# Kernel optimization log

Hardware: AMD Instinct MI355X
Metric: run time of the kernel (lower is better)

Reference implementation:

```python
import jax, jax.numpy as jnp
import numpy as np

D_Z, D_X, K, T = 128, 64, 16, 2048
JITTER = 1e-4
# Tsit5 Butcher tableau. diffrax.diffeqsolve with the default ConstantStepSize
# controller and dt0 = t_curr - t_prev takes exactly ONE Tsit5 step per interval,
# so a single explicit Tsit5 step reproduces the original math.
A21 = 0.161
A31, A32 = -0.008480655492356989, 0.335480655492357
A41, A42, A43 = 2.8971530571054935, -6.359448489975075, 4.3622954328695815
A51, A52, A53, A54 = 5.325864828439257, -11.748883564062828, 7.4955393428898365, -0.09249506636175525
A61, A62, A63, A64, A65 = 5.86145544294642, -12.92096931784711, 8.159367898576159, -0.071584973281401, -0.028269050394068383
B1, B2, B3, B4, B5, B6 = 0.09646076681806523, 0.01, 0.4798896504144996, 1.379008574103742, -3.290069515436081, 2.324710524099774


def setup_inputs() -> dict:
    key = jax.random.key(0)
    ks = jax.random.split(key, 8)
    xs = jax.random.normal(ks[0], (T, D_X), jnp.float32)
    ts = jnp.arange(T, dtype=jnp.float32) * 0.01  # strictly increasing observation times
    expected_s = jax.nn.softmax(jax.random.normal(ks[1], (T, K), jnp.float32), axis=-1)
    mu_0 = jax.random.normal(ks[2], (D_Z,), jnp.float32)
    P_0 = jnp.eye(D_Z, dtype=jnp.float32)
    # stable continuous dynamics: small random part, negative diagonal shift
    A_s = 0.02 * jax.random.normal(ks[3], (K, D_Z, D_Z), jnp.float32) - 0.5 * jnp.eye(D_Z, dtype=jnp.float32)
    b_s = 0.1 * jax.random.normal(ks[4], (K, D_Z), jnp.float32)
    Q_s_chol = 0.1 + 0.1 * jax.random.uniform(ks[5], (K, D_Z), dtype=jnp.float32)
    C = jax.random.normal(ks[6], (D_X, D_Z), jnp.float32) / jnp.sqrt(jnp.float32(D_Z))
    R = 0.1 * jnp.eye(D_X, dtype=jnp.float32)
    return dict(xs=xs, ts=ts, expected_s=expected_s, mu_0=mu_0, P_0=P_0,
                A_s=A_s, b_s=b_s, Q_s_chol=Q_s_chol, C=C, R=R)


def _ode_func(state, s_prob, A_s, b_s, Q_s_chol):
    # state packs [mu (D_Z), P.flatten() (D_Z*D_Z)]
    mu, P = state[:D_Z], state[D_Z:].reshape(D_Z, D_Z)
    w = s_prob / jnp.sum(s_prob)  # jnp.average(..., weights=s_prob) semantics
    drift = jnp.einsum('k,kij,j->i', w, A_s, mu) + w @ b_s
    eA = jnp.einsum('k,kij->ij', w, A_s)
    eQ = jnp.diag(w @ (Q_s_chol ** 2))  # weighted avg of diag(Q_chol)^2
    dP = eA @ P + P @ eA.T + eQ
    return jnp.concatenate([drift, dP.reshape(-1)])


def _kf_update(mu, P, x, C, R):
    y = x - C @ mu
    S = C @ P @ C.T + R + JITTER * jnp.eye(R.shape[0], dtype=P.dtype)
    cho = jax.scipy.linalg.cho_factor(S)
    Kg = jax.scipy.linalg.cho_solve(cho, C @ P).T
    mu_u = mu + Kg @ y
    P_u = P - Kg @ C @ P
    return mu_u, 0.5 * (P_u + P_u.T)


def reference(xs, ts, expected_s, mu_0, P_0, A_s, b_s, Q_s_chol, C, R):
    mu0u, P0u = _kf_update(mu_0, P_0, xs[0], C, R)

    def step(carry, inp):
        mu_prev, P_prev, t_prev = carry
        x, t, s = inp
        y0 = jnp.concatenate([mu_prev, P_prev.reshape(-1)])
        f = lambda st: _ode_func(st, s, A_s, b_s, Q_s_chol)

        def integrate(_):
            h = t - t_prev
            k1 = f(y0)
            k2 = f(y0 + h * (A21 * k1))
            k3 = f(y0 + h * (A31 * k1 + A32 * k2))
            k4 = f(y0 + h * (A41 * k1 + A42 * k2 + A43 * k3))
            k5 = f(y0 + h * (A51 * k1 + A52 * k2 + A53 * k3 + A54 * k4))
            k6 = f(y0 + h * (A61 * k1 + A62 * k2 + A63 * k3 + A64 * k4 + A65 * k5))
            return y0 + h * (B1 * k1 + B2 * k2 + B3 * k3 + B4 * k4 + B5 * k5 + B6 * k6)

        state_pred = jax.lax.cond(t > t_prev, integrate, lambda _: y0, None)
        mu_pr, P_pr = state_pred[:D_Z], state_pred[D_Z:].reshape(D_Z, D_Z)
        mu_u, P_u = _kf_update(mu_pr, P_pr, x, C, R)
        return (mu_u, P_u, t), (mu_u, P_u)

    _, (mu_f, P_f) = jax.lax.scan(step, (mu0u, P0u, ts[0]), (xs[1:], ts[1:], expected_s[1:]))
    mu_filt = jnp.concatenate([mu0u[None], mu_f], axis=0)  # (T, D_Z)
    P_filt = jnp.concatenate([P0u[None], P_f], axis=0)  # (T, D_Z, D_Z)
    return mu_filt, P_filt
```

## Files before the change

### kernel.cpp

```cpp
#include <hip/hip_runtime.h>
#include <math.h>

#define DZ 128
#define DX 64
#define KMIX 16
#define JITTER_C 1e-4f
#define MS (DZ*DZ)
#define ESZ (4*MS + 2*DZ)
#define NCH 256
#define NT 1024
#define SCN (5*MS + 256)

#define SP   0
#define SX   (1*MS)
#define SX2  (2*MS)
#define SX2T (3*MS)
#define SQ   (4*MS)

template<int M, int N, int K, int MODE, bool DUAL>
__device__ void mm_(const float* __restrict__ At, const float* __restrict__ B,
                    float* __restrict__ out, const float* __restrict__ aux,
                    float* __restrict__ outT, float e1 = 0.f)
{
    __syncthreads();
    const int tid = threadIdx.x;
    constexpr int TM = M/32, TN = N/32;
    const int tx = tid & 31, ty = tid >> 5;
    const int i0 = ty*TM, j0 = tx*TN;
    float acc[TM*TN];
#pragma unroll
    for (int e = 0; e < TM*TN; ++e) acc[e] = 0.f;
    auto body = [&](int k) {
        const float* ar = At + k*M + i0;
        const float* br = B + k*N + j0;
        float av[TM], bv[TN];
        if constexpr (TM == 2) {
            float2 t = *reinterpret_cast<const float2*>(ar);
            av[0]=t.x; av[1]=t.y;
        } else {
#pragma unroll
            for (int a = 0; a < TM; a += 4) {
                float4 t = *reinterpret_cast<const float4*>(ar + a);
                av[a]=t.x; av[a+1]=t.y; av[a+2]=t.z; av[a+3]=t.w;
            }
        }
        if constexpr (TN == 2) {
            float2 t = *reinterpret_cast<const float2*>(br);
            bv[0]=t.x; bv[1]=t.y;
        } else {
#pragma unroll
            for (int b = 0; b < TN; b += 4) {
                float4 t = *reinterpret_cast<const float4*>(br + b);
                bv[b]=t.x; bv[b+1]=t.y; bv[b+2]=t.z; bv[b+3]=t.w;
            }
        }
#pragma unroll
        for (int a = 0; a < TM; ++a)
#pragma unroll
            for (int b = 0; b < TN; ++b)
                acc[a*TN+b] = fmaf(av[a], bv[b], acc[a*TN+b]);
    };
    const int off = (tid >> 6) * (K >> 4);
#pragma unroll 8
    for (int k = off; k < K; ++k) body(k);
#pragma unroll 8
    for (int k = 0; k < off; ++k) body(k);
#pragma unroll
    for (int a = 0; a < TM; ++a) {
#pragma unroll
        for (int b = 0; b < TN; ++b) {
            const int row = i0+a, col = j0+b;
            const int idx = row*N + col;
            float v = acc[a*TN+b];
            if constexpr (MODE == 1) v += out[idx];
            else if constexpr (MODE == 2) v = aux[idx] - v;
            else if constexpr (MODE == 3) v += aux[idx];
            else if constexpr (MODE == 4) { v += e1*aux[idx]; if (row==col) v += 1.f; }
            out[idx] = v;
            acc[a*TN+b] = v;
        }
    }
    if constexpr (DUAL) {
#pragma unroll
        for (int b = 0; b < TN; ++b) {
#pragma unroll
            for (int a = 0; a < TM; a += 4) {
                float4 v = make_float4(acc[(a)*TN+b], acc[(a+1)*TN+b], acc[(a+2)*TN+b], acc[(a+3)*TN+b]);
                *reinterpret_cast<float4*>(outT + (j0+b)*M + i0 + a) = v;
            }
        }
    }
    __syncthreads();
}

template<int M, int K, int MODE>
__device__ void mv_(const float* __restrict__ At, const float* __restrict__ v,
                    float* __restrict__ out, const float* __restrict__ aux)
{
    __syncthreads();
    const int tid = threadIdx.x;
    constexpr int TPR = NT / M;
    constexpr int CH  = K / TPR;
    const int r  = tid / TPR;
    const int sg = tid % TPR;
    const int k0 = sg * CH;
    float s = 0.f;
#pragma unroll
    for (int k = 0; k < CH; ++k)
        s = fmaf(At[(k0 + k)*M + r], v[k0 + k], s);
#pragma unroll
    for (int o = 1; o < TPR; o <<= 1) s += __shfl_xor(s, o);
    if (sg == 0) {
        float rr;
        if constexpr (MODE == 0) rr = s;
        else if constexpr (MODE == 1) rr = aux[r] + s;
        else rr = aux[r] - s;
        out[r] = rr;
    }
    __syncthreads();
}

__device__ void trans_g(const float* __restrict__ src, float* __restrict__ dst,
                        float* __restrict__ Lb)
{
    __syncthreads();
    for (int e = threadIdx.x; e < MS; e += NT) {
        int i = e >> 7, j = e & 127;
        Lb[(i << 7) + (j ^ (i & 31))] = src[e];
    }
    __syncthreads();
    for (int e = threadIdx.x; e < MS; e += NT) {
        int a = e >> 7, b = e & 127;
        dst[e] = Lb[(b << 7) + (a ^ (b & 31))];
    }
    __syncthreads();
}

__device__ void gj64_spd(float* __restrict__ A, float* __restrict__ st)
{
    const int tid = threadIdx.x;
    for (int p = 0; p < DX; p += 4) {
        __syncthreads();
        if (tid < 64) {
#pragma unroll
            for (int b = 0; b < 4; ++b) st[tid*4+b] = A[tid*DX + p + b];
        } else if (tid < 128) {
            int j = tid - 64;
#pragma unroll
            for (int b = 0; b < 4; ++b) st[256 + b*64 + j] = A[(p+b)*DX + j];
        }
        __syncthreads();
        float Dm[16], Di[16];
#pragma unroll
        for (int a = 0; a < 4; ++a)
#pragma unroll
            for (int b = 0; b < 4; ++b) {
                Dm[a*4+b] = st[(p+a)*4 + b];
                Di[a*4+b] = (a==b) ? 1.f : 0.f;
            }
#pragma unroll
        for (int q = 0; q < 4; ++q) {
            float rp = 1.f / Dm[q*4+q];
#pragma unroll
            for (int j = 0; j < 4; ++j) { Dm[q*4+j] *= rp; Di[q*4+j] *= rp; }
#pragma unroll
            for (int i = 0; i < 4; ++i) {
                if (i == q) continue;
                float f = Dm[i*4+q];
#pragma unroll
                for (int j = 0; j < 4; ++j) { Dm[i*4+j] = fmaf(-f, Dm[q*4+j], Dm[i*4+j]); Di[i*4+j] = fmaf(-f, Di[q*4+j], Di[i*4+j]); }
            }
        }
        for (int e = tid; e < DX*DX; e += NT) {
            const int i = e >> 6, j = e & 63;
            const bool iP = (i >= p) && (i < p+4);
            const bool jP = (j >= p) && (j < p+4);
            float o;
            if (iP && jP) {
                o = Di[(i-p)*4 + (j-p)];
            } else if (iP) {
                const int a = i - p;
                o = Di[a*4+0]*st[256+0*64+j] + Di[a*4+1]*st[256+1*64+j]
                  + Di[a*4+2]*st[256+2*64+j] + Di[a*4+3]*st[256+3*64+j];
            } else {
                float Ei[4];
#pragma unroll
                for (int b = 0; b < 4; ++b)
                    Ei[b] = st[i*4+0]*Di[0*4+b] + st[i*4+1]*Di[1*4+b]
                          + st[i*4+2]*Di[2*4+b] + st[i*4+3]*Di[3*4+b];
                if (jP) o = -Ei[j-p];
                else    o = A[e] - (Ei[0]*st[256+0*64+j] + Ei[1]*st[256+1*64+j]
                                  + Ei[2]*st[256+2*64+j] + Ei[3]*st[256+3*64+j]);
            }
            A[e] = o;
        }
    }
    __syncthreads();
}

__device__ void gj128_piv(float* __restrict__ A, float* __restrict__ pc, float* __restrict__ pr,
                          int* __restrict__ rec, int* __restrict__ ipv1)
{
    __syncthreads();
    const int tid = threadIdx.x;
    for (int p = 0; p < DZ; ++p) {
        if (tid < 64) {
            float best = -1.f; int bi = p;
            for (int i = tid; i < DZ; i += 64) {
                float v = (i >= p) ? fabsf(A[i*DZ + p]) : -2.f;
                if (v > best) { best = v; bi = i; }
            }
            for (int off = 32; off > 0; off >>= 1) {
                float ob = __shfl_xor(best, off);
                int obi = __shfl_xor(bi, off);
                if (ob > best) { best = ob; bi = obi; }
            }
            if (tid == 0) { rec[p] = bi; ipv1[0] = bi; }
        }
        __syncthreads();
        const int r = ipv1[0];
        if (r != p) {
            for (int j = tid; j < DZ; j += NT) { float t = A[p*DZ+j]; A[p*DZ+j] = A[r*DZ+j]; A[r*DZ+j] = t; }
            __syncthreads();
        }
        if (tid < DZ) { pc[tid] = A[tid*DZ + p]; pr[tid] = A[p*DZ + tid]; }
        __syncthreads();
        const float rp = 1.f / pr[p];
        for (int e = tid; e < MS; e += NT) {
            const int i = e >> 7, j = e & 127;
            const float pv = pr[j] * rp;
            float o;
            if (i == p) o = (j == p) ? rp : pv;
            else { const float fc = pc[i]; o = (j == p) ? (-fc*rp) : (A[e] - fc*pv); }
            A[e] = o;
        }
        __syncthreads();
    }
    for (int p = DZ - 1; p >= 0; --p) {
        const int r = rec[p];
        if (r != p) {
            for (int i = tid; i < DZ; i += NT) { float t = A[i*DZ+p]; A[i*DZ+p] = A[i*DZ+r]; A[i*DZ+r] = t; }
            __syncthreads();
        }
    }
    __syncthreads();
}

__device__ void phase1_dev(int k,
    const float* __restrict__ A_s, const float* __restrict__ b_s,
    const float* __restrict__ Qch, const float* __restrict__ es, const float* __restrict__ ts,
    float* sx, float* sx2, float* sx2t, float* sq,
    float* L0, float* L1,
    float* W16, float* ebv, float* eqv, float* vvv, float* cvec,
    float g1, float g2, float g3, float g4)
{
    const int tid = threadIdx.x;
    const float h = ts[k] - ts[k-1];
    if (h <= 0.f) {
        __syncthreads();
        for (int e = tid; e < MS; e += NT) {
            int i = e >> 7, j = e & 127;
            L0[e] = (i==j) ? 1.f : 0.f;
            sq[e] = 0.f;
        }
        if (tid < DZ) cvec[tid] = 0.f;
        __syncthreads();
        return;
    }
    __syncthreads();
    if (tid < KMIX) W16[tid] = es[(size_t)k*KMIX + tid];
    __syncthreads();
    if (tid == 0) {
        float s = 0.f;
        for (int m = 0; m < KMIX; ++m) s += W16[m];
        float inv = 1.f/s;
        for (int m = 0; m < KMIX; ++m) W16[m] *= inv;
    }
    __syncthreads();
    if (tid < DZ) {
        float eb = 0.f, eq = 0.f;
        for (int m = 0; m < KMIX; ++m) {
            float wm = W16[m];
            eb = fmaf(wm, b_s[m*DZ+tid], eb);
            float qc = Qch[m*DZ+tid];
            eq = fmaf(wm, qc*qc, eq);
        }
        ebv[tid] = eb; eqv[tid] = eq;
    }
    const int tx = tid & 31, ty = tid >> 5;
    const int i0 = ty*4, j0 = tx*4;
    float t16[16];
#pragma unroll
    for (int e = 0; e < 16; ++e) t16[e] = 0.f;
    {
        const int mq = (tid >> 6) & (KMIX - 1);
        for (int mi = 0; mi < KMIX; ++mi) {
            int m = mi + mq; if (m >= KMIX) m -= KMIX;
            float wm = W16[m];
            const float* Am = A_s + (size_t)m * MS;
#pragma unroll
            for (int a = 0; a < 4; ++a) {
                float4 p0 = *reinterpret_cast<const float4*>(&Am[(i0+a)*DZ + j0]);
                t16[a*4+0]=fmaf(wm,p0.x,t16[a*4+0]); t16[a*4+1]=fmaf(wm,p0.y,t16[a*4+1]);
                t16[a*4+2]=fmaf(wm,p0.z,t16[a*4+2]); t16[a*4+3]=fmaf(wm,p0.w,t16[a*4+3]);
            }
        }
    }
#pragma unroll
    for (int a = 0; a < 4; ++a)
#pragma unroll
        for (int b = 0; b < 4; ++b) {
            float v = h * t16[a*4+b];
            L1[(i0+a)*DZ + (j0+b)] = v;
            sx[(i0+a)*DZ + (j0+b)] = v;
            L0[(j0+b)*DZ + (i0+a)] = v;
        }
    __syncthreads();
    {
        float gg[5]; gg[1]=g1; gg[2]=g2; gg[3]=g3; gg[4]=g4;
        if (tid < DZ) vvv[tid] = ebv[tid];
        float creg = (tid < DZ) ? g1 * ebv[tid] : 0.f;
        __syncthreads();
        for (int m = 1; m <= 3; ++m) {
            float vn = 0.f;
            if (tid < DZ)
                for (int kk = 0; kk < DZ; ++kk)
                    vn = fmaf(L0[kk*DZ + tid], vvv[kk], vn);
            __syncthreads();
            if (tid < DZ) vvv[tid] = vn;
            creg = fmaf(gg[m+1], vn, creg);
            __syncthreads();
        }
        if (tid < DZ) cvec[tid] = h * creg;
    }
    mm_<128,128,128,0,true>(L0, L1, sx2, nullptr, sx2t);
    for (int e = tid; e < MS; e += NT) {
        int j = e >> 7, i = e & 127;
        float xt = L0[e];
        float w1  = g2*sx[e] + g3*sx2[e];
        float w1t = g2*xt    + g3*sx2t[e];
        float vq = w1*eqv[i] + eqv[j]*w1t;
        if (i == j) vq += g1*eqv[j];
        sq[e] = h * vq;
        L1[e] = g3*xt + ((i==j) ? g2 : 0.f);
    }
    __syncthreads();
    mm_<128,128,128,4,false>(sx2, L1, L0, L0, nullptr, g1);
}

#define SHARED_DECLS \
    __shared__ __align__(16) float L0[MS]; \
    __shared__ __align__(16) float L1[MS]; \
    __shared__ __align__(16) float SL[DX*DX]; \
    __shared__ __align__(16) float GJB[520]; \
    __shared__ float V0[DZ],V1[DZ],V2[DZ],V3[DZ],V4[DZ],V5[DZ]; \
    __shared__ float r64s[DX], u64s[DX]; \
    __shared__ float W16[KMIX], ebv[DZ], eqv[DZ], vvv[DZ], cvec[DZ]; \
    __shared__ float GJc[DZ], GJr[DZ]; \
    __shared__ int REC[DZ]; __shared__ int IPV1[1];

__global__ __launch_bounds__(NT) void kf_prep(
    const float* __restrict__ Cm, const float* __restrict__ Rm,
    const float* __restrict__ mu0, const float* __restrict__ P0,
    const float* __restrict__ xs,
    float* Ct, float* Rj, float* Rji, float* mu0u, float* p0u, float* scr)
{
    SHARED_DECLS
    const int tid = threadIdx.x;
    for (int i = tid; i < DZ*DX; i += NT) { int z = i>>6, m = i&63; Ct[i] = Cm[m*DZ + z]; }
    for (int i = tid; i < DX*DX; i += NT) {
        int a = i>>6, b = i&63;
        float v = Rm[i] + ((a==b) ? JITTER_C : 0.f);
        Rj[i] = v; SL[i] = v;
    }
    gj64_spd(SL, GJB);
    for (int i = tid; i < DX*DX; i += NT) Rji[i] = SL[i];
    float* z  = scr + SX;
    float* cp = scr + SX + DZ*DX;
    float* kt = scr + SX2;
    mm_<128,64,128,0,true>(P0, Ct, z, nullptr, cp);
    mm_<64,64,128,3,false>(Ct, z, SL, Rj, nullptr);
    gj64_spd(SL, GJB);
    mm_<64,128,64,0,false>(SL, cp, kt, nullptr, nullptr);
    mv_<64,128,2>(Ct, mu0, r64s, xs);
    mv_<128,64,1>(kt, r64s, mu0u, mu0);
    mm_<128,128,64,2,false>(kt, cp, p0u, P0, nullptr);
    __syncthreads();
    for (int e = tid; e < MS; e += NT) L0[e] = p0u[e];
    __syncthreads();
    for (int e = tid; e < MS; e += NT) {
        int i = e>>7, j = e&127;
        p0u[e] = 0.5f * (L0[e] + L0[j*DZ + i]);
    }
}

__global__ __launch_bounds__(NT) void kf_passA(
    const float* __restrict__ A_s, const float* __restrict__ b_s,
    const float* __restrict__ Qch, const float* __restrict__ es,
    const float* __restrict__ ts, const float* __restrict__ xs,
    const float* __restrict__ Ct, const float* __restrict__ Rj,
    const float* __restrict__ Rji,
    const float* __restrict__ mu0u, const float* __restrict__ p0u,
    float* elems, float* scr, int T, int LCH,
    float g1, float g2, float g3, float g4)
{
    SHARED_DECLS
    const int c = blockIdx.x, tid = threadIdx.x;
    float* sc = scr + (size_t)c * SCN;
    float* R = elems + (size_t)c * ESZ;
    float* RAs = R; float* RAts = R+MS; float* RCs = R+2*MS; float* RJs = R+3*MS;
    float* Rbs = R+4*MS; float* Rhs = R+4*MS+DZ;
    int eBeg = c*LCH, eEnd = (c*LCH + LCH < T) ? (c*LCH + LCH) : T;
    if (eBeg >= eEnd && c != 0) {
        for (int e = tid; e < MS; e += NT) {
            int i = e>>7, j = e&127; float id = (i==j)?1.f:0.f;
            RAs[e]=id; RAts[e]=id; RCs[e]=0.f; RJs[e]=0.f;
        }
        if (tid < DZ) { Rbs[tid]=0.f; Rhs[tid]=0.f; }
        return;
    }
    if (c == 0) {
        for (int e = tid; e < MS; e += NT) { RAs[e]=0.f; RCs[e]=p0u[e]; RJs[e]=0.f; }
        if (tid < DZ) { V0[tid]=mu0u[tid]; V5[tid]=0.f; }
        eBeg = 1;
    } else {
        for (int e = tid; e < MS; e += NT) {
            int i = e>>7, j = e&127;
            RAs[e] = (i==j)?1.f:0.f; RCs[e]=0.f; RJs[e]=0.f;
        }
        if (tid < DZ) { V0[tid]=0.f; V5[tid]=0.f; }
    }
    __syncthreads();
    float* sx = sc+SX; float* sx2 = sc+SX2; float* sx2t = sc+SX2T; float* sq = sc+SQ;
    float* z  = L0;    float* zt = L0 + 8192;
    float* y  = sq;    float* hh = sq + 8192;
    float* h2 = sx;
    for (int e = eBeg; e < eEnd; ++e) {
        phase1_dev(e, A_s,b_s,Qch,es,ts, sx,sx2,sx2t,sq, L0,L1,
                   W16,ebv,eqv,vvv,cvec, g1,g2,g3,g4);
        mm_<128,128,128,0,false>(L0, RAs, sx, nullptr, nullptr);
        mv_<128,128,1>(L0, V0, V1, cvec);
        mm_<128,128,128,0,false>(RCs, L0, sx2, nullptr, nullptr);
        mm_<128,128,128,3,false>(L0, sx2, L1, sq, nullptr);
        mm_<128,64,128,0,true>(L1, Ct, z, nullptr, zt);
        mm_<64,64,128,3,false>(Ct, z, SL, Rj, nullptr);
        gj64_spd(SL, GJB);
        mm_<64,128,128,0,false>(Ct, sx, y, nullptr, nullptr);
        mm_<64,128,64,0,false>(SL, y, hh, nullptr, nullptr);
        mm_<128,128,64,2,false>(zt, hh, RAs, sx, nullptr);
        mm_<128,128,64,1,false>(y, hh, RJs, nullptr, nullptr);
        mm_<64,128,64,0,false>(SL, zt, h2, nullptr, nullptr);
        mm_<128,128,64,2,false>(zt, h2, RCs, L1, nullptr);
        mv_<64,128,2>(Ct, V1, r64s, xs + (size_t)e*DX);
        mv_<64,64,0>(Rji, xs + (size_t)e*DX, u64s, nullptr);
        mv_<128,64,1>(zt, u64s, V2, V1);
        mv_<64,128,0>(Ct, V2, GJc, nullptr);
        mv_<64,64,0>(SL, GJc, GJr, nullptr);
        mv_<128,64,2>(zt, GJr, V0, V2);
        mv_<64,64,0>(SL, r64s, u64s, nullptr);
        mv_<128,64,1>(y, u64s, V5, V5);
    }
    __syncthreads();
    if (tid < DZ) { Rbs[tid] = V0[tid]; Rhs[tid] = V5[tid]; }
    trans_g(RAs, RAts, L0);
}

__device__ void combine(float* Rd,
    const float* EA, const float* EAt, const float* EC, const float* EJ,
    const float* Ebg, const float* Ehg,
    float* t2, float* t3,
    float* L0, float* L1,
    float* V0, float* V1, float* V2, float* V3, float* V4, float* V5,
    float* GJc, float* GJr, int* REC, int* IPV1, int lastj)
{
    float* RA = Rd; float* RAt = Rd+MS; float* RC = Rd+2*MS; float* RJ = Rd+3*MS;
    float* Rb = Rd+4*MS; float* Rh = Rd+4*MS+DZ;
    const int tid = threadIdx.x;
    __syncthreads();
    if (tid < DZ) { V0[tid]=Ebg[tid]; V1[tid]=Ehg[tid]; V2[tid]=Rb[tid]; }
    mm_<128,128,128,0,false>(EJ, RC, L0, nullptr, nullptr);
    if (tid < DZ) L0[tid*DZ + tid] += 1.f;
    gj128_piv(L0, GJc, GJr, REC, IPV1);
    if (!lastj) {
        mm_<128,128,128,0,false>(L0, RA, L1, nullptr, nullptr);
        mm_<128,128,128,0,false>(EJ, RA, t2, nullptr, nullptr);
        mm_<128,128,128,1,false>(L1, t2, RJ, nullptr, nullptr);
        mv_<128,128,2>(EJ, V2, V4, V1);
        mv_<128,128,1>(L1, V4, Rh, Rh);
    }
    mv_<128,128,1>(RC, V1, V3, V2);
    mv_<128,128,0>(L0, V3, V5, nullptr);
    mv_<128,128,1>(EAt, V5, Rb, V0);
    mm_<128,128,128,0,false>(L0, RC, t3, nullptr, nullptr);
    mm_<128,128,128,0,false>(t3, EAt, t2, nullptr, nullptr);
    mm_<128,128,128,3,false>(EAt, t2, RC, EC, nullptr);
    if (!lastj) {
        mm_<128,128,128,0,false>(EAt, L1, RA, nullptr, nullptr);
        trans_g(RA, RAt, L1);
    }
}

__global__ __launch_bounds__(NT) void kf_scan(
    const float* __restrict__ in, float* __restrict__ out, float* scr, int r, int lastj)
{
    SHARED_DECLS
    const int c = blockIdx.x;
    float* sc = scr + (size_t)c * SCN;
    float* dst = out + (size_t)c * ESZ;
    const float* src = in + (size_t)((c >= r) ? (c - r) : c) * ESZ;
    if (lastj) {
        for (int e = threadIdx.x; e < MS; e += NT) dst[2*MS + e] = src[2*MS + e];
        for (int e = threadIdx.x; e < DZ; e += NT) dst[4*MS + e] = src[4*MS + e];
    } else {
        for (int e = threadIdx.x; e < ESZ; e += NT) dst[e] = src[e];
    }
    if (c >= r) {
        const float* E = in + (size_t)c * ESZ;
        combine(dst, E, E+MS, E+2*MS, E+3*MS, E+4*MS, E+4*MS+DZ,
                sc+SP, sc+SX, L0, L1,
                V0,V1,V2,V3,V4,V5, GJc, GJr, REC, IPV1, lastj);
    }
}

__global__ __launch_bounds__(NT) void kf_passC(
    const float* __restrict__ A_s, const float* __restrict__ b_s,
    const float* __restrict__ Qch, const float* __restrict__ es,
    const float* __restrict__ ts, const float* __restrict__ xs,
    const float* __restrict__ Ct, const float* __restrict__ Rj,
    const float* __restrict__ mu0u, const float* __restrict__ p0u,
    const float* __restrict__ pfx,
    float* mu_out, float* P_out, float* scr, int T, int LCH,
    float g1, float g2, float g3, float g4)
{
    SHARED_DECLS
    const int c = blockIdx.x, tid = threadIdx.x;
    float* sc = scr + (size_t)c * SCN;
    float* P = sc + SP;
    int eBeg = c*LCH, eEnd = (c*LCH + LCH < T) ? (c*LCH + LCH) : T;
    if (eBeg >= eEnd && c != 0) return;
    if (c == 0) {
        for (int e = tid; e < MS; e += NT) { float v = p0u[e]; P[e] = v; P_out[e] = v; }
        if (tid < DZ) { V0[tid] = mu0u[tid]; mu_out[tid] = mu0u[tid]; }
        eBeg = 1;
    } else {
        const float* X = pfx + (size_t)(c-1) * ESZ;
        for (int e = tid; e < MS; e += NT) P[e] = X[2*MS + e];
        if (tid < DZ) V0[tid] = X[4*MS + tid];
    }
    __syncthreads();
    float* sx = sc+SX; float* sx2 = sc+SX2; float* sx2t = sc+SX2T; float* sq = sc+SQ;
    float* z  = L0;    float* zt = L0 + 8192;
    for (int e = eBeg; e < eEnd; ++e) {
        phase1_dev(e, A_s,b_s,Qch,es,ts, sx,sx2,sx2t,sq, L0,L1,
                   W16,ebv,eqv,vvv,cvec, g1,g2,g3,g4);
        mm_<128,128,128,0,false>(P, L0, sx, nullptr, nullptr);
        mm_<128,128,128,3,false>(L0, sx, L1, sq, nullptr);
        mv_<128,128,1>(L0, V0, V1, cvec);
        mm_<128,64,128,0,true>(L1, Ct, z, nullptr, zt);
        mm_<64,64,128,3,false>(Ct, z, SL, Rj, nullptr);
        gj64_spd(SL, GJB);
        mm_<64,128,64,0,false>(SL, zt, sx2, nullptr, nullptr);
        mv_<64,128,2>(Ct, V1, r64s, xs + (size_t)e*DX);
        mv_<128,64,1>(sx2, r64s, V0, V1);
        if (tid < DZ) mu_out[(size_t)e*DZ + tid] = V0[tid];
        mm_<128,128,64,2,false>(zt, sx2, L1, L1, nullptr);
        for (int ee = tid; ee < MS; ee += NT) {
            int i = ee >> 7, j = ee & 127;
            L0[(i << 7) + (j ^ (i & 31))] = L1[ee];
        }
        __syncthreads();
        float* po = P_out + (size_t)e * MS;
        for (int ee = tid; ee < MS; ee += NT) {
            int i = ee >> 7, j = ee & 127;
            float v = 0.5f * (L1[ee] + L0[(j << 7) + (i ^ (j & 31))]);
            P[ee] = v;
            __builtin_nontemporal_store(v, &po[ee]);
        }
        __syncthreads();
    }
}

static void compute_gamma(double g[7])
{
    const double A[6][5] = {
        {0, 0, 0, 0, 0},
        {0.161, 0, 0, 0, 0},
        {-0.008480655492356989, 0.335480655492357, 0, 0, 0},
        {2.8971530571054935, -6.359448489975075, 4.3622954328695815, 0, 0},
        {5.325864828439257, -11.748883564062828, 7.4955393428898365, -0.09249506636175525, 0},
        {5.86145544294642, -12.92096931784711, 8.159367898576159, -0.071584973281401, -0.028269050394068383}};
    const double B[6] = {0.09646076681806523, 0.01, 0.4798896504144996,
                         1.379008574103742, -3.290069515436081, 2.324710524099774};
    double e[6][6];
    for (int i = 0; i < 6; ++i)
        for (int d = 0; d < 6; ++d) e[i][d] = 0.0;
    for (int i = 0; i < 6; ++i) {
        e[i][0] = 1.0;
        for (int j = 0; j < i; ++j)
            for (int d = 0; d < 5; ++d)
                e[i][d + 1] += A[i][j] * e[j][d];
    }
    g[0] = 1.0;
    for (int m = 1; m <= 6; ++m) {
        double s = 0.0;
        for (int i = 0; i < 6; ++i) s += B[i] * e[i][m - 1];
        g[m] = s;
    }
}

extern "C" void kernel_launch(void* const* d_in, const int* in_sizes, int n_in,
                              void* d_out, int out_size, void* d_ws, size_t ws_size,
                              hipStream_t stream)
{
    const float* xs  = (const float*)d_in[0];
    const float* ts  = (const float*)d_in[1];
    const float* es  = (const float*)d_in[2];
    const float* mu0 = (const float*)d_in[3];
    const float* P0  = (const float*)d_in[4];
    const float* A_s = (const float*)d_in[5];
    const float* b_s = (const float*)d_in[6];
    const float* Qch = (const float*)d_in[7];
    const float* Cm  = (const float*)d_in[8];
    const float* Rm  = (const float*)d_in[9];
    const int T = in_sizes[1];

    float* mu_out = (float*)d_out;
    float* P_out  = mu_out + (size_t)T * DZ;

    float* ws = (float*)d_ws;
    float* Ct    = ws;
    float* Rj    = ws + 8192;
    float* Rji   = ws + 12288;
    float* mu0u  = ws + 16384;
    float* p0u   = ws + 16512;
    float* elemsA = ws + 32896;
    float* elemsB = elemsA + (size_t)NCH * ESZ;
    float* scr    = elemsB + (size_t)NCH * ESZ;

    const int LCH = (T + NCH - 1) / NCH;

    double g[7];
    compute_gamma(g);
    const float g1 = (float)g[1], g2 = (float)g[2], g3 = (float)g[3], g4 = (float)g[4];

    hipLaunchKernelGGL(kf_prep, dim3(1), dim3(NT), 0, stream,
                       Cm, Rm, mu0, P0, xs, Ct, Rj, Rji, mu0u, p0u, scr);
    hipLaunchKernelGGL(kf_passA, dim3(NCH), dim3(NT), 0, stream,
                       A_s, b_s, Qch, es, ts, xs, Ct, Rj, Rji, mu0u, p0u,
                       elemsA, scr, T, LCH, g1, g2, g3, g4);
    float* bufs[2] = {elemsA, elemsB};
    int cur = 0;
    for (int r = 1; r < NCH; r <<= 1) {
        const int lastj = ((r << 1) >= NCH) ? 1 : 0;
        hipLaunchKernelGGL(kf_scan, dim3(NCH), dim3(NT), 0, stream,
                           bufs[cur], bufs[cur ^ 1], scr, r, lastj);
        cur ^= 1;
    }
    hipLaunchKernelGGL(kf_passC, dim3(NCH), dim3(NT), 0, stream,
                       A_s, b_s, Qch, es, ts, xs, Ct, Rj, mu0u, p0u,
                       bufs[cur], mu_out, P_out, scr, T, LCH, g1, g2, g3, g4);
}
```

Measured before the change: 11.66 ms.

## Precompute per-step mixed dynamics matrices in bf16 and shrink scratch footprint

Adds two pre-kernels. One normalises the mixture weights and step sizes once per step. The other precomputes h*sum_k w_k A_k for every time step and stores it as bf16, so passA and passC load a packed matrix instead of re-reducing 16 fp32 matrices from A_s. Scratch per chunk drops from five matrices to three, passC reuses the spare ping-pong buffer as scratch, and combine in the scan writes directly to its destination instead of copying first. The bf16 rounding of the dynamics matrix lowers precision and may hurt accuracy, and the extra precompute pass writes T*MS halves to global memory.

Measured after the change: 11.97 ms. 1.03x slower.

```diff
diff --git a/kernel.cpp b/kernel.cpp
--- a/kernel.cpp
+++ b/kernel.cpp
@@ -9,13 +9,10 @@
 #define ESZ (4*MS + 2*DZ)
 #define NCH 256
 #define NT 1024
-#define SCN (5*MS + 256)
-
-#define SP   0
-#define SX   (1*MS)
-#define SX2  (2*MS)
-#define SX2T (3*MS)
-#define SQ   (4*MS)
+#define SCN (3*MS + 256)
+
+typedef unsigned short ushortT;
+typedef unsigned int uintT;
 
 template<int M, int N, int K, int MODE, bool DUAL>
 __device__ void mm_(const float* __restrict__ At, const float* __restrict__ B,
@@ -247,35 +244,29 @@
 }
 
 __device__ void phase1_dev(int k,
-    const float* __restrict__ A_s, const float* __restrict__ b_s,
-    const float* __restrict__ Qch, const float* __restrict__ es, const float* __restrict__ ts,
-    float* sx, float* sx2, float* sx2t, float* sq,
+    const ushortT* __restrict__ Xb, const float* __restrict__ hbuf,
+    const float* __restrict__ wn,
+    const float* __restrict__ b_s, const float* __restrict__ Qch,
+    float* s1, float* s2, float* s3,
     float* L0, float* L1,
     float* W16, float* ebv, float* eqv, float* vvv, float* cvec,
     float g1, float g2, float g3, float g4)
 {
     const int tid = threadIdx.x;
-    const float h = ts[k] - ts[k-1];
+    const float h = hbuf[k];
     if (h <= 0.f) {
         __syncthreads();
         for (int e = tid; e < MS; e += NT) {
             int i = e >> 7, j = e & 127;
             L0[e] = (i==j) ? 1.f : 0.f;
-            sq[e] = 0.f;
+            s3[e] = 0.f;
         }
         if (tid < DZ) cvec[tid] = 0.f;
         __syncthreads();
         return;
     }
     __syncthreads();
-    if (tid < KMIX) W16[tid] = es[(size_t)k*KMIX + tid];
-    __syncthreads();
-    if (tid == 0) {
-        float s = 0.f;
-        for (int m = 0; m < KMIX; ++m) s += W16[m];
-        float inv = 1.f/s;
-        for (int m = 0; m < KMIX; ++m) W16[m] *= inv;
-    }
+    if (tid < KMIX) W16[tid] = wn[(size_t)k*KMIX + tid];
     __syncthreads();
     if (tid < DZ) {
         float eb = 0.f, eq = 0.f;
@@ -287,34 +278,23 @@
         }
         ebv[tid] = eb; eqv[tid] = eq;
     }
-    const int tx = tid & 31, ty = tid >> 5;
-    const int i0 = ty*4, j0 = tx*4;
-    float t16[16];
-#pragma unroll
-    for (int e = 0; e < 16; ++e) t16[e] = 0.f;
     {
-        const int mq = (tid >> 6) & (KMIX - 1);
-        for (int mi = 0; mi < KMIX; ++mi) {
-            int m = mi + mq; if (m >= KMIX) m -= KMIX;
-            float wm = W16[m];
-            const float* Am = A_s + (size_t)m * MS;
-#pragma unroll
-            for (int a = 0; a < 4; ++a) {
-                float4 p0 = *reinterpret_cast<const float4*>(&Am[(i0+a)*DZ + j0]);
-                t16[a*4+0]=fmaf(wm,p0.x,t16[a*4+0]); t16[a*4+1]=fmaf(wm,p0.y,t16[a*4+1]);
-                t16[a*4+2]=fmaf(wm,p0.z,t16[a*4+2]); t16[a*4+3]=fmaf(wm,p0.w,t16[a*4+3]);
-            }
-        }
-    }
-#pragma unroll
-    for (int a = 0; a < 4; ++a)
-#pragma unroll
-        for (int b = 0; b < 4; ++b) {
-            float v = h * t16[a*4+b];
-            L1[(i0+a)*DZ + (j0+b)] = v;
-            sx[(i0+a)*DZ + (j0+b)] = v;
-            L0[(j0+b)*DZ + (i0+a)] = v;
-        }
+        const uint4* xr = reinterpret_cast<const uint4*>(Xb + (size_t)k*MS);
+        for (int e8 = tid; e8 < MS/8; e8 += NT) {
+            uint4 pk = xr[e8];
+            int base = e8*8; int i = base >> 7; int j = base & 127;
+            uintT uu[4] = {pk.x, pk.y, pk.z, pk.w};
+#pragma unroll
+            for (int t = 0; t < 4; ++t) {
+                float lo = __uint_as_float(uu[t] << 16);
+                float hi = __uint_as_float(uu[t] & 0xFFFF0000u);
+                L1[base + 2*t]     = lo;
+                L1[base + 2*t + 1] = hi;
+                L0[(j + 2*t)*DZ + i]     = lo;
+                L0[(j + 2*t + 1)*DZ + i] = hi;
+            }
+        }
+    }
     __syncthreads();
     {
         float gg[5]; gg[1]=g1; gg[2]=g2; gg[3]=g3; gg[4]=g4;
@@ -333,19 +313,20 @@
         }
         if (tid < DZ) cvec[tid] = h * creg;
     }
-    mm_<128,128,128,0,true>(L0, L1, sx2, nullptr, sx2t);
+    mm_<128,128,128,0,true>(L0, L1, s1, nullptr, s2);
     for (int e = tid; e < MS; e += NT) {
         int j = e >> 7, i = e & 127;
+        float xe = L1[e];
         float xt = L0[e];
-        float w1  = g2*sx[e] + g3*sx2[e];
-        float w1t = g2*xt    + g3*sx2t[e];
+        float w1  = g2*xe + g3*s1[e];
+        float w1t = g2*xt + g3*s2[e];
         float vq = w1*eqv[i] + eqv[j]*w1t;
         if (i == j) vq += g1*eqv[j];
-        sq[e] = h * vq;
+        s3[e] = h * vq;
         L1[e] = g3*xt + ((i==j) ? g2 : 0.f);
     }
     __syncthreads();
-    mm_<128,128,128,4,false>(sx2, L1, L0, L0, nullptr, g1);
+    mm_<128,128,128,4,false>(s1, L1, L0, L0, nullptr, g1);
 }
 
 #define SHARED_DECLS \
@@ -359,6 +340,55 @@
     __shared__ float GJc[DZ], GJr[DZ]; \
     __shared__ int REC[DZ]; __shared__ int IPV1[1];
 
+__global__ __launch_bounds__(256) void kf_wprep(
+    const float* __restrict__ es, const float* __restrict__ ts,
+    float* __restrict__ wn, float* __restrict__ hbuf, int T)
+{
+    int k = blockIdx.x*256 + threadIdx.x;
+    if (k >= T) return;
+    float w[KMIX]; float s = 0.f;
+    for (int m = 0; m < KMIX; ++m) { w[m] = es[(size_t)k*KMIX+m]; s += w[m]; }
+    float inv = 1.f/s;
+    for (int m = 0; m < KMIX; ++m) wn[(size_t)k*KMIX+m] = w[m]*inv;
+    hbuf[k] = (k >= 1) ? (ts[k]-ts[k-1]) : 0.f;
+}
+
+__global__ __launch_bounds__(NT) void kf_xprep(
+    const float* __restrict__ A_s, const float* __restrict__ wn,
+    const float* __restrict__ hbuf, ushortT* __restrict__ Xb, int T)
+{
+    __shared__ float Al[16*8*128];
+    __shared__ float wloc[KMIX];
+    const int tid = threadIdx.x;
+    const int rt = blockIdx.x & 15, sg = blockIdx.x >> 4;
+    const int r0 = rt*8;
+    for (int i4 = tid; i4 < 4096; i4 += NT) {
+        int m = i4 >> 8, rem = i4 & 255;
+        int r = rem >> 5, c4 = rem & 31;
+        float4 v = *reinterpret_cast<const float4*>(A_s + (size_t)m*MS + (size_t)(r0+r)*DZ + c4*4);
+        *reinterpret_cast<float4*>(&Al[m*1024 + r*128 + c4*4]) = v;
+    }
+    __syncthreads();
+    const int spg = (T + 15) >> 4;
+    int k0 = sg*spg; int k1 = k0 + spg; if (k1 > T) k1 = T;
+    if (k0 < 1) k0 = 1;
+    const int rr = tid >> 7, col = tid & 127;
+    for (int k = k0; k < k1; ++k) {
+        if (tid < KMIX) wloc[tid] = wn[(size_t)k*KMIX + tid];
+        __syncthreads();
+        float hk = hbuf[k];
+        float s = 0.f;
+#pragma unroll
+        for (int m = 0; m < KMIX; ++m)
+            s = fmaf(wloc[m], Al[m*1024 + rr*128 + col], s);
+        float v = hk * s;
+        uintT u = __float_as_uint(v);
+        u += 0x7FFFu + ((u >> 16) & 1u);
+        Xb[(size_t)k*MS + (size_t)(r0+rr)*DZ + col] = (ushortT)(u >> 16);
+        __syncthreads();
+    }
+}
+
 __global__ __launch_bounds__(NT) void kf_prep(
     const float* __restrict__ Cm, const float* __restrict__ Rm,
     const float* __restrict__ mu0, const float* __restrict__ P0,
@@ -375,9 +405,9 @@
     }
     gj64_spd(SL, GJB);
     for (int i = tid; i < DX*DX; i += NT) Rji[i] = SL[i];
-    float* z  = scr + SX;
-    float* cp = scr + SX + DZ*DX;
-    float* kt = scr + SX2;
+    float* z  = scr;
+    float* cp = scr + DZ*DX;
+    float* kt = scr + MS;
     mm_<128,64,128,0,true>(P0, Ct, z, nullptr, cp);
     mm_<64,64,128,3,false>(Ct, z, SL, Rj, nullptr);
     gj64_spd(SL, GJB);
@@ -395,12 +425,13 @@
 }
 
 __global__ __launch_bounds__(NT) void kf_passA(
-    const float* __restrict__ A_s, const float* __restrict__ b_s,
-    const float* __restrict__ Qch, const float* __restrict__ es,
-    const float* __restrict__ ts, const float* __restrict__ xs,
+    const float* __restrict__ xs,
     const float* __restrict__ Ct, const float* __restrict__ Rj,
     const float* __restrict__ Rji,
     const float* __restrict__ mu0u, const float* __restrict__ p0u,
+    const float* __restrict__ b_s, const float* __restrict__ Qch,
+    const float* __restrict__ wn, const float* __restrict__ hbuf,
+    const ushortT* __restrict__ Xb,
     float* elems, float* scr, int T, int LCH,
     float g1, float g2, float g3, float g4)
 {
@@ -431,26 +462,24 @@
         if (tid < DZ) { V0[tid]=0.f; V5[tid]=0.f; }
     }
     __syncthreads();
-    float* sx = sc+SX; float* sx2 = sc+SX2; float* sx2t = sc+SX2T; float* sq = sc+SQ;
+    float* s1 = sc; float* s2 = sc + MS; float* s3 = sc + 2*MS;
     float* z  = L0;    float* zt = L0 + 8192;
-    float* y  = sq;    float* hh = sq + 8192;
-    float* h2 = sx;
     for (int e = eBeg; e < eEnd; ++e) {
-        phase1_dev(e, A_s,b_s,Qch,es,ts, sx,sx2,sx2t,sq, L0,L1,
-                   W16,ebv,eqv,vvv,cvec, g1,g2,g3,g4);
-        mm_<128,128,128,0,false>(L0, RAs, sx, nullptr, nullptr);
+        phase1_dev(e, Xb, hbuf, wn, b_s, Qch, s1, s2, s3, L0, L1,
+                   W16, ebv, eqv, vvv, cvec, g1, g2, g3, g4);
+        mm_<128,128,128,0,false>(L0, RAs, s2, nullptr, nullptr);
         mv_<128,128,1>(L0, V0, V1, cvec);
-        mm_<128,128,128,0,false>(RCs, L0, sx2, nullptr, nullptr);
-        mm_<128,128,128,3,false>(L0, sx2, L1, sq, nullptr);
+        mm_<128,128,128,0,false>(RCs, L0, s1, nullptr, nullptr);
+        mm_<128,128,128,3,false>(L0, s1, L1, s3, nullptr);
         mm_<128,64,128,0,true>(L1, Ct, z, nullptr, zt);
         mm_<64,64,128,3,false>(Ct, z, SL, Rj, nullptr);
         gj64_spd(SL, GJB);
-        mm_<64,128,128,0,false>(Ct, sx, y, nullptr, nullptr);
-        mm_<64,128,64,0,false>(SL, y, hh, nullptr, nullptr);
-        mm_<128,128,64,2,false>(zt, hh, RAs, sx, nullptr);
-        mm_<128,128,64,1,false>(y, hh, RJs, nullptr, nullptr);
-        mm_<64,128,64,0,false>(SL, zt, h2, nullptr, nullptr);
-        mm_<128,128,64,2,false>(zt, h2, RCs, L1, nullptr);
+        mm_<64,128,128,0,false>(Ct, s2, s3, nullptr, nullptr);
+        mm_<64,128,64,0,false>(SL, s3, s3 + 8192, nullptr, nullptr);
+        mm_<128,128,64,2,false>(zt, s3 + 8192, RAs, s2, nullptr);
+        mm_<128,128,64,1,false>(s3, s3 + 8192, RJs, nullptr, nullptr);
+        mm_<64,128,64,0,false>(SL, zt, s2, nullptr, nullptr);
+        mm_<128,128,64,2,false>(zt, s2, RCs, L1, nullptr);
         mv_<64,128,2>(Ct, V1, r64s, xs + (size_t)e*DX);
         mv_<64,64,0>(Rji, xs + (size_t)e*DX, u64s, nullptr);
         mv_<128,64,1>(zt, u64s, V2, V1);
@@ -458,46 +487,47 @@
         mv_<64,64,0>(SL, GJc, GJr, nullptr);
         mv_<128,64,2>(zt, GJr, V0, V2);
         mv_<64,64,0>(SL, r64s, u64s, nullptr);
-        mv_<128,64,1>(y, u64s, V5, V5);
+        mv_<128,64,1>(s3, u64s, V5, V5);
     }
     __syncthreads();
     if (tid < DZ) { Rbs[tid] = V0[tid]; Rhs[tid] = V5[tid]; }
     trans_g(RAs, RAts, L0);
 }
 
-__device__ void combine(float* Rd,
-    const float* EA, const float* EAt, const float* EC, const float* EJ,
-    const float* Ebg, const float* Ehg,
-    float* t2, float* t3,
-    float* L0, float* L1,
+__device__ void combine(float* D, const float* Rsrc, const float* E,
+    float* sa, float* L0, float* L1,
     float* V0, float* V1, float* V2, float* V3, float* V4, float* V5,
     float* GJc, float* GJr, int* REC, int* IPV1, int lastj)
 {
-    float* RA = Rd; float* RAt = Rd+MS; float* RC = Rd+2*MS; float* RJ = Rd+3*MS;
-    float* Rb = Rd+4*MS; float* Rh = Rd+4*MS+DZ;
+    const float* RA_s = Rsrc;            const float* RC_s = Rsrc + 2*MS;
+    const float* RJ_s = Rsrc + 3*MS;
+    const float* Rb_s = Rsrc + 4*MS;     const float* Rh_s = Rsrc + 4*MS + DZ;
+    const float* EAt  = E + MS;          const float* EC   = E + 2*MS;
+    const float* EJ   = E + 3*MS;
+    const float* Ebg  = E + 4*MS;        const float* Ehg  = E + 4*MS + DZ;
+    float* D_RA = D; float* D_RAt = D+MS; float* D_RC = D+2*MS; float* D_RJ = D+3*MS;
+    float* D_Rb = D+4*MS; float* D_Rh = D+4*MS+DZ;
     const int tid = threadIdx.x;
     __syncthreads();
-    if (tid < DZ) { V0[tid]=Ebg[tid]; V1[tid]=Ehg[tid]; V2[tid]=Rb[tid]; }
-    mm_<128,128,128,0,false>(EJ, RC, L0, nullptr, nullptr);
+    if (tid < DZ) { V0[tid]=Ebg[tid]; V1[tid]=Ehg[tid]; V2[tid]=Rb_s[tid]; }
+    mm_<128,128,128,0,false>(EJ, RC_s, L0, nullptr, nullptr);
     if (tid < DZ) L0[tid*DZ + tid] += 1.f;
     gj128_piv(L0, GJc, GJr, REC, IPV1);
     if (!lastj) {
-        mm_<128,128,128,0,false>(L0, RA, L1, nullptr, nullptr);
-        mm_<128,128,128,0,false>(EJ, RA, t2, nullptr, nullptr);
-        mm_<128,128,128,1,false>(L1, t2, RJ, nullptr, nullptr);
+        mm_<128,128,128,0,false>(L0, RA_s, L1, nullptr, nullptr);
+        mm_<128,128,128,0,false>(EJ, RA_s, sa, nullptr, nullptr);
+        mm_<128,128,128,3,false>(L1, sa, D_RJ, RJ_s, nullptr);
         mv_<128,128,2>(EJ, V2, V4, V1);
-        mv_<128,128,1>(L1, V4, Rh, Rh);
-    }
-    mv_<128,128,1>(RC, V1, V3, V2);
+        mv_<128,128,1>(L1, V4, D_Rh, Rh_s);
+        mm_<128,128,128,0,false>(EAt, L1, D_RA, nullptr, nullptr);
+        trans_g(D_RA, D_RAt, L1);
+    }
+    mv_<128,128,1>(RC_s, V1, V3, V2);
     mv_<128,128,0>(L0, V3, V5, nullptr);
-    mv_<128,128,1>(EAt, V5, Rb, V0);
-    mm_<128,128,128,0,false>(L0, RC, t3, nullptr, nullptr);
-    mm_<128,128,128,0,false>(t3, EAt, t2, nullptr, nullptr);
-    mm_<128,128,128,3,false>(EAt, t2, RC, EC, nullptr);
-    if (!lastj) {
-        mm_<128,128,128,0,false>(EAt, L1, RA, nullptr, nullptr);
-        trans_g(RA, RAt, L1);
-    }
+    mv_<128,128,1>(EAt, V5, D_Rb, V0);
+    mm_<128,128,128,0,false>(L0, RC_s, L1, nullptr, nullptr);
+    mm_<128,128,128,0,false>(L1, EAt, sa, nullptr, nullptr);
+    mm_<128,128,128,3,false>(EAt, sa, D_RC, EC, nullptr);
 }
 
 __global__ __launch_bounds__(NT) void kf_scan(
@@ -507,35 +537,38 @@
     const int c = blockIdx.x;
     float* sc = scr + (size_t)c * SCN;
     float* dst = out + (size_t)c * ESZ;
-    const float* src = in + (size_t)((c >= r) ? (c - r) : c) * ESZ;
-    if (lastj) {
-        for (int e = threadIdx.x; e < MS; e += NT) dst[2*MS + e] = src[2*MS + e];
-        for (int e = threadIdx.x; e < DZ; e += NT) dst[4*MS + e] = src[4*MS + e];
+    if (c >= r) {
+        const float* Rsrc = in + (size_t)(c - r) * ESZ;
+        const float* E = in + (size_t)c * ESZ;
+        combine(dst, Rsrc, E, sc, L0, L1,
+                V0,V1,V2,V3,V4,V5, GJc, GJr, REC, IPV1, lastj);
     } else {
-        for (int e = threadIdx.x; e < ESZ; e += NT) dst[e] = src[e];
-    }
-    if (c >= r) {
-        const float* E = in + (size_t)c * ESZ;
-        combine(dst, E, E+MS, E+2*MS, E+3*MS, E+4*MS, E+4*MS+DZ,
-                sc+SP, sc+SX, L0, L1,
-                V0,V1,V2,V3,V4,V5, GJc, GJr, REC, IPV1, lastj);
+        const float* src = in + (size_t)c * ESZ;
+        if (lastj) {
+            for (int e = threadIdx.x; e < MS; e += NT) dst[2*MS + e] = src[2*MS + e];
+            for (int e = threadIdx.x; e < DZ; e += NT) dst[4*MS + e] = src[4*MS + e];
+        } else {
+            for (int e = threadIdx.x; e < ESZ; e += NT) dst[e] = src[e];
+        }
     }
 }
 
 __global__ __launch_bounds__(NT) void kf_passC(
-    const float* __restrict__ A_s, const float* __restrict__ b_s,
-    const float* __restrict__ Qch, const float* __restrict__ es,
-    const float* __restrict__ ts, const float* __restrict__ xs,
+    const float* __restrict__ xs,
     const float* __restrict__ Ct, const float* __restrict__ Rj,
     const float* __restrict__ mu0u, const float* __restrict__ p0u,
+    const float* __restrict__ b_s, const float* __restrict__ Qch,
+    const float* __restrict__ wn, const float* __restrict__ hbuf,
+    const ushortT* __restrict__ Xb,
     const float* __restrict__ pfx,
-    float* mu_out, float* P_out, float* scr, int T, int LCH,
+    float* mu_out, float* P_out, float* scrC, int T, int LCH,
     float g1, float g2, float g3, float g4)
 {
     SHARED_DECLS
     const int c = blockIdx.x, tid = threadIdx.x;
-    float* sc = scr + (size_t)c * SCN;
-    float* P = sc + SP;
+    float* sc = scrC + (size_t)c * ESZ;
+    float* P = sc;
+    float* s1 = sc + MS; float* s2 = sc + 2*MS; float* s3 = sc + 3*MS;
     int eBeg = c*LCH, eEnd = (c*LCH + LCH < T) ? (c*LCH + LCH) : T;
     if (eBeg >= eEnd && c != 0) return;
     if (c == 0) {
@@ -548,22 +581,21 @@
         if (tid < DZ) V0[tid] = X[4*MS + tid];
     }
     __syncthreads();
-    float* sx = sc+SX; float* sx2 = sc+SX2; float* sx2t = sc+SX2T; float* sq = sc+SQ;
     float* z  = L0;    float* zt = L0 + 8192;
     for (int e = eBeg; e < eEnd; ++e) {
-        phase1_dev(e, A_s,b_s,Qch,es,ts, sx,sx2,sx2t,sq, L0,L1,
-                   W16,ebv,eqv,vvv,cvec, g1,g2,g3,g4);
-        mm_<128,128,128,0,false>(P, L0, sx, nullptr, nullptr);
-        mm_<128,128,128,3,false>(L0, sx, L1, sq, nullptr);
+        phase1_dev(e, Xb, hbuf, wn, b_s, Qch, s1, s2, s3, L0, L1,
+                   W16, ebv, eqv, vvv, cvec, g1, g2, g3, g4);
+        mm_<128,128,128,0,false>(P, L0, s2, nullptr, nullptr);
+        mm_<128,128,128,3,false>(L0, s2, L1, s3, nullptr);
         mv_<128,128,1>(L0, V0, V1, cvec);
         mm_<128,64,128,0,true>(L1, Ct, z, nullptr, zt);
         mm_<64,64,128,3,false>(Ct, z, SL, Rj, nullptr);
         gj64_spd(SL, GJB);
-        mm_<64,128,64,0,false>(SL, zt, sx2, nullptr, nullptr);
+        mm_<64,128,64,0,false>(SL, zt, s2, nullptr, nullptr);
         mv_<64,128,2>(Ct, V1, r64s, xs + (size_t)e*DX);
-        mv_<128,64,1>(sx2, r64s, V0, V1);
+        mv_<128,64,1>(s2, r64s, V0, V1);
         if (tid < DZ) mu_out[(size_t)e*DZ + tid] = V0[tid];
-        mm_<128,128,64,2,false>(zt, sx2, L1, L1, nullptr);
+        mm_<128,128,64,2,false>(zt, s2, L1, L1, nullptr);
         for (int ee = tid; ee < MS; ee += NT) {
             int i = ee >> 7, j = ee & 127;
             L0[(i << 7) + (j ^ (i & 31))] = L1[ee];
@@ -633,7 +665,10 @@
     float* Rji   = ws + 12288;
     float* mu0u  = ws + 16384;
     float* p0u   = ws + 16512;
-    float* elemsA = ws + 32896;
+    float* wn    = ws + 32896;
+    float* hbuf  = wn + (size_t)T*16;
+    ushortT* Xb  = (ushortT*)(hbuf + T);
+    float* elemsA = (float*)(Xb + (size_t)T*MS);
     float* elemsB = elemsA + (size_t)NCH * ESZ;
     float* scr    = elemsB + (size_t)NCH * ESZ;
 
@@ -643,10 +678,14 @@
     compute_gamma(g);
     const float g1 = (float)g[1], g2 = (float)g[2], g3 = (float)g[3], g4 = (float)g[4];
 
+    hipLaunchKernelGGL(kf_wprep, dim3((T + 255)/256), dim3(256), 0, stream,
+                       es, ts, wn, hbuf, T);
+    hipLaunchKernelGGL(kf_xprep, dim3(256), dim3(NT), 0, stream,
+                       A_s, wn, hbuf, Xb, T);
     hipLaunchKernelGGL(kf_prep, dim3(1), dim3(NT), 0, stream,
                        Cm, Rm, mu0, P0, xs, Ct, Rj, Rji, mu0u, p0u, scr);
     hipLaunchKernelGGL(kf_passA, dim3(NCH), dim3(NT), 0, stream,
-                       A_s, b_s, Qch, es, ts, xs, Ct, Rj, Rji, mu0u, p0u,
+                       xs, Ct, Rj, Rji, mu0u, p0u, b_s, Qch, wn, hbuf, Xb,
                        elemsA, scr, T, LCH, g1, g2, g3, g4);
     float* bufs[2] = {elemsA, elemsB};
     int cur = 0;
@@ -657,6 +696,6 @@
         cur ^= 1;
     }
     hipLaunchKernelGGL(kf_passC, dim3(NCH), dim3(NT), 0, stream,
-                       A_s, b_s, Qch, es, ts, xs, Ct, Rj, mu0u, p0u,
-                       bufs[cur], mu_out, P_out, scr, T, LCH, g1, g2, g3, g4);
-}
+                       xs, Ct, Rj, mu0u, p0u, b_s, Qch, wn, hbuf, Xb,
+                       bufs[cur], mu_out, P_out, bufs[cur ^ 1], T, LCH, g1, g2, g3, g4);
+}
```
